# Kernel optimization log

Measured on AMD Instinct MI355X. Metric: run time of the kernel, lower is better.

Reference implementation:

```python
import jax, jax.numpy as jnp
import numpy as np

B, C, H, W = 16, 512, 32, 32
G = 8  # GroupNorm groups
EPS = 1e-5


def setup_inputs() -> dict:
    key = jax.random.key(0)
    ks = jax.random.split(key, 6)
    s = 1.0 / np.sqrt(C)
    return {
        "x": jax.random.normal(ks[0], (B, C, H, W), jnp.float32),
        "gamma": jnp.ones((C,), jnp.float32),
        "beta": jnp.zeros((C,), jnp.float32),
        "wq": jax.random.normal(ks[1], (C, C), jnp.float32) * s,
        "bq": jnp.zeros((C,), jnp.float32),
        "wk": jax.random.normal(ks[2], (C, C), jnp.float32) * s,
        "bk": jnp.zeros((C,), jnp.float32),
        "wv": jax.random.normal(ks[3], (C, C), jnp.float32) * s,
        "bv": jnp.zeros((C,), jnp.float32),
        "wp": jax.random.normal(ks[4], (C, C), jnp.float32) * s,
        "bp": jnp.zeros((C,), jnp.float32),
    }


def reference(x, gamma, beta, wq, bq, wk, bk, wv, bv, wp, bp):
    b, c, h, w = x.shape
    n = h * w
    # GroupNorm(8, C) over (C//G, H, W) per group
    xg = x.reshape(b, G, c // G, n)
    mean = xg.mean(axis=(2, 3), keepdims=True)
    var = xg.var(axis=(2, 3), keepdims=True)
    xn = ((xg - mean) * jax.lax.rsqrt(var + EPS)).reshape(b, c, n)
    xn = xn * gamma[:, None] + beta[:, None]
    # 1x1 conv projections: [C_out, C_in] @ [B, C_in, N]
    q = jnp.einsum('oc,bcn->bon', wq, xn) + bq[:, None]
    k = jnp.einsum('oc,bcn->bon', wk, xn) + bk[:, None]
    v = jnp.einsum('oc,bcn->bon', wv, xn) + bv[:, None]
    scale = 1.0 / (c ** 0.5)
    attn = jax.nn.softmax(jnp.einsum('bci,bcj->bij', q, k) * scale, axis=-1)
    # out[b,c,i] = sum_j v[b,c,j] * attn[b,i,j]
    out = jnp.einsum('bcj,bij->bci', v, attn)
    out = jnp.einsum('oc,bcn->bon', wp, out) + bp[:, None]
    return x + out.reshape(b, c, h, w)
```

## Files before the change

### kernel.cpp

```cpp
#include <hip/hip_runtime.h>

typedef __attribute__((ext_vector_type(8))) short short8;
typedef __attribute__((ext_vector_type(4))) short short4v;
typedef __attribute__((ext_vector_type(4))) float f32x4;
typedef __attribute__((ext_vector_type(4))) int i32x4;

__device__ __forceinline__ short f2bf(float f) {
  unsigned u = __builtin_bit_cast(unsigned, f);
  u = u + 0x7fffu + ((u >> 16) & 1u);
  return (short)(u >> 16);
}
__device__ __forceinline__ int q8(float v) {
  int q = (int)rintf(v * 16.f);
  return q < -127 ? -127 : (q > 127 ? 127 : q);
}
__device__ __forceinline__ int qw8(float v) {
  int q = (int)rintf(v * 512.f);
  return q < -127 ? -127 : (q > 127 ? 127 : q);
}

__device__ __forceinline__ int xcd_swz() {
  const int cpx = gridDim.x >> 3;
  return (blockIdx.x & 7) * cpx + (blockIdx.x >> 3);
}

__global__ __launch_bounds__(256) void pre_kernel(
    const float* __restrict__ x, float2* __restrict__ part,
    const float* __restrict__ wq, const float* __restrict__ wk,
    const float* __restrict__ wp, const float* __restrict__ wv,
    const float* __restrict__ bv, const float* __restrict__ bp,
    short* __restrict__ wp_bf, short* __restrict__ wvT,
    short* __restrict__ wqT, short* __restrict__ wkT,
    float* __restrict__ bias2, float* __restrict__ lsum,
    float* __restrict__ cadd) {
  const int blk = blockIdx.x, t = threadIdx.x;
  if (blk < 32) {
    const int w = t >> 6, lane = t & 63;
    const float4 b0 = *(const float4*)(bv + lane * 8);
    const float4 b1 = *(const float4*)(bv + lane * 8 + 4);
#pragma unroll
    for (int idx = 0; idx < 4; ++idx) {
      const int m = blk * 16 + w * 4 + idx;
      const float4 a0 = *(const float4*)(wp + (long)m * 512 + lane * 8);
      const float4 a1 = *(const float4*)(wp + (long)m * 512 + lane * 8 + 4);
      float s = a0.x * b0.x + a0.y * b0.y + a0.z * b0.z + a0.w * b0.w
              + a1.x * b1.x + a1.y * b1.y + a1.z * b1.z + a1.w * b1.w;
#pragma unroll
      for (int o = 32; o > 0; o >>= 1) s += __shfl_xor(s, o, 64);
      if (lane == 0) bias2[m] = bp[m] + s;
    }
  } else if (blk < 224) {
    const float* src; short* dst; int t2;
    if (blk < 96)       { t2 = blk - 32;  src = wv; dst = wvT; }
    else if (blk < 160) { t2 = blk - 96;  src = wq; dst = wqT; }
    else                { t2 = blk - 160; src = wk; dst = wkT; }
    const int tr = t2 >> 3, tc = t2 & 7;
    __shared__ float tile[64][65];
    const int r = t >> 2, q4 = t & 3;
    const float* s4 = src + (long)(tr * 64 + r) * 512 + tc * 64 + q4 * 16;
#pragma unroll
    for (int k = 0; k < 4; ++k) {
      float4 v = ((const float4*)s4)[k];
      tile[r][q4 * 16 + k * 4 + 0] = v.x;
      tile[r][q4 * 16 + k * 4 + 1] = v.y;
      tile[r][q4 * 16 + k * 4 + 2] = v.z;
      tile[r][q4 * 16 + k * 4 + 3] = v.w;
    }
    __syncthreads();
    const int oc = t >> 2, seg = t & 3;
    short tmp[16];
#pragma unroll
    for (int e = 0; e < 16; ++e) tmp[e] = f2bf(tile[seg * 16 + e][oc]);
    short* dp = dst + (long)(tc * 64 + oc) * 512 + tr * 64 + seg * 16;
    *(short8*)dp = *(short8*)&tmp[0];
    *(short8*)(dp + 8) = *(short8*)&tmp[8];
  } else if (blk < 228) {
    float4* p = (float4*)lsum;
    const int base = (blk - 224) * 1024 + t * 4;
#pragma unroll
    for (int k = 0; k < 4; ++k) p[base + k] = make_float4(0.f, 0.f, 0.f, 0.f);
  } else if (blk < 232) {
    float4* p = (float4*)cadd;
    const int base = (blk - 228) * 1024 + t * 4;
#pragma unroll
    for (int k = 0; k < 4; ++k) p[base + k] = make_float4(0.f, 0.f, 0.f, 0.f);
  } else if (blk < 488) {
    const int i4 = (blk - 232) * 1024 + t * 4;
    float4 v = *(const float4*)(wp + i4);
    short4v o;
    o.x = f2bf(v.x); o.y = f2bf(v.y); o.z = f2bf(v.z); o.w = f2bf(v.w);
    *(short4v*)(wp_bf + i4) = o;
  } else {
    const int blk2 = blk - 488;
    const float* base = x + (long)blk2 * 8192;
    float s = 0.f, ss = 0.f;
#pragma unroll
    for (int j = 0; j < 8; ++j) {
      float4 v = ((const float4*)base)[t + j * 256];
      s  += v.x + v.y + v.z + v.w;
      ss += v.x * v.x + v.y * v.y + v.z * v.z + v.w * v.w;
    }
    for (int o = 32; o > 0; o >>= 1) { s += __shfl_xor(s, o, 64); ss += __shfl_xor(ss, o, 64); }
    __shared__ float rs[4], rss[4];
    if ((t & 63) == 0) { rs[t >> 6] = s; rss[t >> 6] = ss; }
    __syncthreads();
    if (t == 0) {
      part[blk2] = make_float2(rs[0] + rs[1] + rs[2] + rs[3],
                               rss[0] + rss[1] + rss[2] + rss[3]);
    }
  }
}

#define BM 128
#define BK 64

__device__ __forceinline__ int swz_idx(int row, int k) {
  return row * 64 + ((((k >> 3) ^ row) & 7) << 3) + (k & 7);
}

__device__ __forceinline__ void gemm_core(
    const short* __restrict__ Ab, const short* __restrict__ Bb,
    short* lds, f32x4 (&acc)[4][4], int m0, int n0, int K, int tid) {
  const int lane = tid & 63, w = tid >> 6;
  const int wm = (w >> 1) * 64, wn = (w & 1) * 64;
  const int rowst = w * 32 + (lane >> 3);
  for (int k0 = 0; k0 < K; k0 += BK) {
    __syncthreads();
#pragma unroll
    for (int it = 0; it < 4; ++it) {
      int ci = w * 4 + it;
      int row = rowst + it * 8;
      int slot = (lane & 7) ^ (row & 7);
      const short* ga = Ab + (long)(m0 + row) * K + k0 + slot * 8;
      __builtin_amdgcn_global_load_lds(
          (const __attribute__((address_space(1))) void*)ga,
          (__attribute__((address_space(3))) void*)(lds + ci * 512), 16, 0, 0);
      const short* gb = Bb + (long)(n0 + row) * K + k0 + slot * 8;
      __builtin_amdgcn_global_load_lds(
          (const __attribute__((address_space(1))) void*)gb,
          (__attribute__((address_space(3))) void*)(lds + 8192 + ci * 512), 16, 0, 0);
    }
    __syncthreads();
#pragma unroll
    for (int kk = 0; kk < 2; ++kk) {
      short8 af[4], bf[4];
      const int kf = kk * 32 + (lane >> 4) * 8;
#pragma unroll
      for (int i = 0; i < 4; ++i) {
        af[i] = *(const short8*)(lds + swz_idx(wm + i * 16 + (lane & 15), kf));
        bf[i] = *(const short8*)(lds + 8192 + swz_idx(wn + i * 16 + (lane & 15), kf));
      }
#pragma unroll
      for (int i = 0; i < 4; ++i)
#pragma unroll
        for (int j = 0; j < 4; ++j)
          acc[i][j] = __builtin_amdgcn_mfma_f32_16x16x32_bf16(af[i], bf[j], acc[i][j], 0, 0, 0);
    }
  }
}

__device__ __forceinline__ void gemm_core_i8(
    const char* __restrict__ Ab, const char* __restrict__ Bb,
    char* lds, i32x4 (&acc)[4][4], int m0, int n0, int ldaB, int Kbytes, int tid) {
  const int lane = tid & 63, w = tid >> 6;
  const int wm = (w >> 1) * 64, wn = (w & 1) * 64;
  long aoff[4], boff[4];
  int ldst[4];
#pragma unroll
  for (int it = 0; it < 4; ++it) {
    const int ci = w * 4 + it;
    const int row = ci * 8 + (lane >> 3);
    const int lg = (lane & 7) ^ (row & 7);
    aoff[it] = (long)(m0 + row) * ldaB + lg * 16;
    boff[it] = (long)(n0 + row) * ldaB + lg * 16;
    ldst[it] = ci * 1024 + lane * 16;
  }
  const int ar = lane & 15, g4 = lane >> 4;
  for (int k0 = 0; k0 < Kbytes; k0 += 128) {
    __syncthreads();
#pragma unroll
    for (int it = 0; it < 4; ++it) {
      __builtin_amdgcn_global_load_lds(
          (const __attribute__((address_space(1))) void*)(Ab + aoff[it] + k0),
          (__attribute__((address_space(3))) void*)(lds + ldst[it]), 16, 0, 0);
      __builtin_amdgcn_global_load_lds(
          (const __attribute__((address_space(1))) void*)(Bb + boff[it] + k0),
          (__attribute__((address_space(3))) void*)(lds + 16384 + ldst[it]), 16, 0, 0);
    }
    __syncthreads();
#pragma unroll
    for (int kk = 0; kk < 2; ++kk) {
      i32x4 af[4], bf[4];
#pragma unroll
      for (int i = 0; i < 4; ++i) {
        const int rowA = wm + i * 16 + ar;
        af[i] = *(const i32x4*)(lds + rowA * 128 + (((kk * 4 + g4) ^ (rowA & 7)) * 16));
        const int rowB = wn + i * 16 + ar;
        bf[i] = *(const i32x4*)(lds + 16384 + rowB * 128 + (((kk * 4 + g4) ^ (rowB & 7)) * 16));
      }
#pragma unroll
      for (int i = 0; i < 4; ++i)
#pragma unroll
        for (int j = 0; j < 4; ++j)
          acc[i][j] = __builtin_amdgcn_mfma_i32_16x16x64_i8(af[i], bf[j], acc[i][j], 0, 0, 0);
    }
  }
}

__device__ __forceinline__ void gemm_core_fp8(
    const char* __restrict__ Ab, const char* __restrict__ Bb,
    char* lds, f32x4 (&acc)[4][4], int m0, int n0, int ldaB, int Kbytes, int tid) {
  const int lane = tid & 63, w = tid >> 6;
  const int wm = (w >> 1) * 64, wn = (w & 1) * 64;
  long aoff[4], boff[4];
  int ldst[4];
#pragma unroll
  for (int it = 0; it < 4; ++it) {
    const int ci = w * 4 + it;
    const int row = ci * 8 + (lane >> 3);
    const int lg = (lane & 7) ^ (row & 7);
    aoff[it] = (long)(m0 + row) * ldaB + lg * 16;
    boff[it] = (long)(n0 + row) * ldaB + lg * 16;
    ldst[it] = ci * 1024 + lane * 16;
  }
  const int ar = lane & 15, g4 = lane >> 4;
  const int gsel = g4 >> 1, hsel = (g4 & 1) * 8;
  for (int k0 = 0; k0 < Kbytes; k0 += 128) {
    __syncthreads();
#pragma unroll
    for (int it = 0; it < 4; ++it) {
      __builtin_amdgcn_global_load_lds(
          (const __attribute__((address_space(1))) void*)(Ab + aoff[it] + k0),
          (__attribute__((address_space(3))) void*)(lds + ldst[it]), 16, 0, 0);
      __builtin_amdgcn_global_load_lds(
          (const __attribute__((address_space(1))) void*)(Bb + boff[it] + k0),
          (__attribute__((address_space(3))) void*)(lds + 16384 + ldst[it]), 16, 0, 0);
    }
    __syncthreads();
#pragma unroll
    for (int c = 0; c < 4; ++c) {
      long af[4], bf[4];
#pragma unroll
      for (int i = 0; i < 4; ++i) {
        const int rowA = wm + i * 16 + ar;
        af[i] = *(const long*)(lds + rowA * 128 + (((2 * c + gsel) ^ (rowA & 7)) * 16) + hsel);
        const int rowB = wn + i * 16 + ar;
        bf[i] = *(const long*)(lds + 16384 + rowB * 128 + (((2 * c + gsel) ^ (rowB & 7)) * 16) + hsel);
      }
#pragma unroll
      for (int i = 0; i < 4; ++i)
#pragma unroll
        for (int j = 0; j < 4; ++j)
          acc[i][j] = __builtin_amdgcn_mfma_f32_16x16x32_fp8_fp8(af[i], bf[j], acc[i][j], 0, 0, 0);
    }
  }
}

__global__ __launch_bounds__(256, 3) void wgemm_kernel(
    const short* __restrict__ wqT, const short* __restrict__ wkT,
    const short* __restrict__ wp_bf, const short* __restrict__ wvT,
    const float* __restrict__ bq, char* __restrict__ Wst_i8,
    float* __restrict__ v1) {
  __shared__ short lds[2 * BM * BK];
  const int y = blockIdx.y, tid = threadIdx.x;
  if (y < 8) {
    const int which = y >> 2;
    const short* A  = which ? wp_bf : wqT;
    const short* Bt = which ? wvT   : wkT;
    const int m0 = (y & 3) * 128, n0 = blockIdx.x * 128;
    f32x4 acc[4][4] = {};
    gemm_core(A, Bt, lds, acc, m0, n0, 512, tid);
    const int lane = tid & 63, w = tid >> 6;
    const int wm = (w >> 1) * 64, wn = (w & 1) * 64;
    const int mb = m0 + wm + (lane >> 4) * 4;
    const int nb = n0 + wn + (lane & 15);
    char* C = Wst_i8 + which * 262144;
#pragma unroll
    for (int i = 0; i < 4; ++i)
#pragma unroll
      for (int r = 0; r < 4; ++r) {
        int m = mb + i * 16 + r;
#pragma unroll
        for (int j = 0; j < 4; ++j)
          C[(long)m * 512 + nb + j * 16] = (char)qw8(acc[i][j][r]);
      }
  } else {
    const int w = tid >> 6, lane = tid & 63;
    const int base_r = ((y - 8) * 4 + blockIdx.x) * 64;
    const float4 b0 = *(const float4*)(bq + lane * 8);
    const float4 b1 = *(const float4*)(bq + lane * 8 + 4);
#pragma unroll
    for (int idx = 0; idx < 16; ++idx) {
      const int c = base_r + w * 16 + idx;
      const short8 a = *(const short8*)(wkT + (long)c * 512 + lane * 8);
      float av[8];
#pragma unroll
      for (int e = 0; e < 8; ++e)
        av[e] = __builtin_bit_cast(float, ((unsigned)(unsigned short)a[e]) << 16);
      float s = av[0] * b0.x + av[1] * b0.y + av[2] * b0.z + av[3] * b0.w
              + av[4] * b1.x + av[5] * b1.y + av[6] * b1.z + av[7] * b1.w;
#pragma unroll
      for (int o = 32; o > 0; o >>= 1) s += __shfl_xor(s, o, 64);
      if (lane == 0) v1[c] = s;
    }
  }
}

#define TP 133
__global__ __launch_bounds__(256) void gn_norm_t(
    const float* __restrict__ x, const float2* __restrict__ part,
    const float* __restrict__ gamma, const float* __restrict__ beta,
    const float* __restrict__ v1, char* __restrict__ xi8,
    float* __restrict__ cadd) {
  const int blk = blockIdx.x;
  const int nc = blk & 7, g = (blk >> 3) & 7, b = blk >> 6;
  const int t = threadIdx.x;
  float s = 0.f, ss = 0.f;
#pragma unroll
  for (int j = 0; j < 8; ++j) {
    float2 p = part[(b * 8 + g) * 8 + j];
    s += p.x; ss += p.y;
  }
  const float mean = s * (1.f / 65536.f);
  const float var  = ss * (1.f / 65536.f) - mean * mean;
  const float rstd = rsqrtf(var + 1e-5f);

  const float* base = x + (long)(b * 512 + g * 64) * 1024 + nc * 128;
  __shared__ float tile[64][TP];
  const int row = t >> 2, c4 = t & 3;
#pragma unroll
  for (int j = 0; j < 8; ++j) {
    float4 v = *(const float4*)(base + (long)row * 1024 + (c4 + j * 4) * 4);
    *(float4*)&tile[row][(c4 + j * 4) * 4] = v;
  }
  const int cl4 = (t & 15) * 4;
  float ga[4], be[4];
#pragma unroll
  for (int j = 0; j < 4; ++j) {
    float gm = gamma[g * 64 + cl4 + j];
    ga[j] = gm * rstd;
    be[j] = beta[g * 64 + cl4 + j] - mean * ga[j];
  }
  const float4 v1c = *(const float4*)(v1 + g * 64 + cl4);
  __syncthreads();
  char* qb = xi8 + (long)b * 524288 + (long)(nc * 128) * 512 + g * 64 + cl4;
  float* cb = cadd + b * 1024 + nc * 128;
#pragma unroll
  for (int it = 0; it < 8; ++it) {
    const int tok = (t >> 4) + it * 16;
    float x0 = tile[cl4 + 0][tok] * ga[0] + be[0];
    float x1 = tile[cl4 + 1][tok] * ga[1] + be[1];
    float x2 = tile[cl4 + 2][tok] * ga[2] + be[2];
    float x3 = tile[cl4 + 3][tok] * ga[3] + be[3];
    unsigned pk = (q8(x0) & 255) | ((q8(x1) & 255) << 8)
                | ((q8(x2) & 255) << 16) | ((q8(x3) & 255) << 24);
    *(unsigned*)(qb + (long)tok * 512) = pk;
    float p = v1c.x * x0 + v1c.y * x1 + v1c.z * x2 + v1c.w * x3;
    p += __shfl_xor(p, 1, 64); p += __shfl_xor(p, 2, 64);
    p += __shfl_xor(p, 4, 64); p += __shfl_xor(p, 8, 64);
    if ((t & 15) == 0) atomicAdd(&cb[tok], p);
  }
}

__global__ __launch_bounds__(256, 3) void zu_gemm(
    const char* __restrict__ Wst_i8, const char* __restrict__ xi,
    char* __restrict__ zi, char* __restrict__ u8) {
  __shared__ char lds[32768];
  const int lw = xcd_swz();
  const int b = lw >> 6, rem = lw & 63, y = rem >> 3, xg = rem & 7;
  const int which = y >> 2;
  const int m0 = y * 128;
  const int mloc0 = m0 - which * 512;
  const int n0 = xg * 128;
  const char* Bb = xi + (long)b * 524288;
  const int tid = threadIdx.x, lane = tid & 63;
  i32x4 acc[4][4] = {};
  gemm_core_i8(Wst_i8, Bb, lds, acc, m0, n0, 512, 512, tid);

  const int w = tid >> 6;
  const int wm = (w >> 1) * 64, wn = (w & 1) * 64;
  const int mb = mloc0 + wm + (lane >> 4) * 4;
  const int nb = n0 + wn + (lane & 15);
  const float dq = 1.f / 8192.f;
  if (which == 0) {
    char* C = zi + (long)b * 524288;
#pragma unroll
    for (int i = 0; i < 4; ++i) {
      int m = mb + i * 16;
#pragma unroll
      for (int j = 0; j < 4; ++j) {
        int n = nb + j * 16;
        unsigned pk = (q8((float)acc[i][j][0] * dq) & 255)
                    | ((q8((float)acc[i][j][1] * dq) & 255) << 8)
                    | ((q8((float)acc[i][j][2] * dq) & 255) << 16)
                    | ((q8((float)acc[i][j][3] * dq) & 255) << 24);
        *(unsigned*)(C + (long)n * 512 + m) = pk;
      }
    }
  } else {
    char* C = u8 + (long)b * 524288;
#pragma unroll
    for (int i = 0; i < 4; ++i) {
#pragma unroll
      for (int r = 0; r < 4; ++r) {
        int m = mb + i * 16 + r;
#pragma unroll
        for (int j = 0; j < 4; ++j) {
          int n = nb + j * 16;
          float v = (float)acc[i][j][r] * dq;
          int pk = __builtin_amdgcn_cvt_pk_fp8_f32(v, v, 0, false);
          C[(long)m * 1024 + n] = (char)(pk & 255);
        }
      }
    }
  }
}

__global__ __launch_bounds__(256, 3) void sexp_i8(
    const char* __restrict__ zi, const char* __restrict__ xi,
    char* __restrict__ P8, float* __restrict__ lsum,
    const float* __restrict__ cadd, float scale) {
  __shared__ char lds[32768];
  const int lw = xcd_swz();
  const int b = lw >> 6, rem = lw & 63;
  const int m0 = (rem >> 3) * 128, n0 = (rem & 7) * 128;
  const char* Ab = zi + (long)b * 524288;
  const char* Bb = xi + (long)b * 524288;
  const int tid = threadIdx.x, lane = tid & 63, w = tid >> 6;
  const int wm = (w >> 1) * 64, wn = (w & 1) * 64;
  i32x4 acc[4][4] = {};
  gemm_core_i8(Ab, Bb, lds, acc, m0, n0, 512, 512, tid);

  const int ar = lane & 15, g4 = lane >> 4;
  const int mb = m0 + wm + g4 * 4;
  const int nb = n0 + wn + ar;
  char* C = P8 + (long)b * 1048576;
  float4 ca[4];
#pragma unroll
  for (int i = 0; i < 4; ++i)
    ca[i] = *(const float4*)(cadd + b * 1024 + mb + i * 16);
  float rowsum[4] = {0.f, 0.f, 0.f, 0.f};
  const float qs = 1.f / 256.f;
#pragma unroll
  for (int j = 0; j < 4; ++j) {
    int n = nb + j * 16;
#pragma unroll
    for (int i = 0; i < 4; ++i) {
      int m = mb + i * 16;
      float e0 = __expf(((float)acc[i][j][0] * qs + ca[i].x) * scale);
      float e1 = __expf(((float)acc[i][j][1] * qs + ca[i].y) * scale);
      float e2 = __expf(((float)acc[i][j][2] * qs + ca[i].z) * scale);
      float e3 = __expf(((float)acc[i][j][3] * qs + ca[i].w) * scale);
      rowsum[j] += (e0 + e1) + (e2 + e3);
      int pk = __builtin_amdgcn_cvt_pk_fp8_f32(e0, e1, 0, false);
      pk = __builtin_amdgcn_cvt_pk_fp8_f32(e2, e3, pk, true);
      *(unsigned*)(C + (long)n * 1024 + m) = (unsigned)pk;
    }
  }
#pragma unroll
  for (int j = 0; j < 4; ++j) {
    rowsum[j] += __shfl_xor(rowsum[j], 16, 64);
    rowsum[j] += __shfl_xor(rowsum[j], 32, 64);
  }
  if (lane < 16) {
#pragma unroll
    for (int j = 0; j < 4; ++j)
      atomicAdd(&lsum[b * 1024 + nb + j * 16], rowsum[j]);
  }
}

__global__ __launch_bounds__(256, 3) void out_fp8(
    const char* __restrict__ u8, const char* __restrict__ P8,
    float* __restrict__ out, const float* __restrict__ bias2,
    const float* __restrict__ x, const float* __restrict__ lsum) {
  __shared__ char lds[32768];
  const int lw = xcd_swz();
  const int b = lw >> 5, rem = lw & 31;
  const int m0 = (rem >> 3) * 128, n0 = (rem & 7) * 128;
  const char* Ab = u8 + (long)b * 524288;
  const char* Bb = P8 + (long)b * 1048576;
  const int tid = threadIdx.x, lane = tid & 63, w = tid >> 6;
  const int wm = (w >> 1) * 64, wn = (w & 1) * 64;
  f32x4 acc[4][4] = {};
  gemm_core_fp8(Ab, Bb, lds, acc, m0, n0, 1024, 1024, tid);

  const int ar = lane & 15, g4 = lane >> 4;
  const int mb = m0 + wm + g4 * 4;
  const int nb = n0 + wn + ar;
  float* C = out + (long)b * 524288;
  const float* R = x + (long)b * 524288;
#pragma unroll
  for (int j = 0; j < 4; ++j) {
    int n = nb + j * 16;
    float rl = 1.0f / lsum[b * 1024 + n];
#pragma unroll
    for (int i = 0; i < 4; ++i) {
#pragma unroll
      for (int r = 0; r < 4; ++r) {
        int m = mb + i * 16 + r;
        C[(long)m * 1024 + n] = acc[i][j][r] * rl + bias2[m] + R[(long)m * 1024 + n];
      }
    }
  }
}

extern "C" void kernel_launch(void* const* d_in, const int* in_sizes, int n_in,
                              void* d_out, int out_size, void* d_ws, size_t ws_size,
                              hipStream_t stream) {
  const float* x     = (const float*)d_in[0];
  const float* gamma = (const float*)d_in[1];
  const float* beta  = (const float*)d_in[2];
  const float* wq    = (const float*)d_in[3];
  const float* bq    = (const float*)d_in[4];
  const float* wk    = (const float*)d_in[5];
  const float* bk    = (const float*)d_in[6];
  const float* wv    = (const float*)d_in[7];
  const float* bv    = (const float*)d_in[8];
  const float* wp    = (const float*)d_in[9];
  const float* bp    = (const float*)d_in[10];
  (void)bk;

  char* ws = (char*)d_ws;
  char*  Wst_i8 = (char*)ws;
  float* bias2 = (float*)(ws + 1572864l);
  float* lsum  = (float*)(ws + 1638400l);
  float* v1    = (float*)(ws + 1703936l);
  float* cadd  = (float*)(ws + 1708032l);
  char*  z_i8  = (char*)(ws + 18874368l);
  char*  x_i8  = (char*)(ws + 35651584l);
  char*  u_f8  = (char*)(ws + 52428800l);
  char*  P8    = (char*)(ws + 69206016l);
  float2* gnpart = (float2*)P8;
  short* wp_bf = (short*)(P8 + 131072);
  short* wvT   = (short*)(P8 + 655360);
  short* wqT   = (short*)(P8 + 1179648);
  short* wkT   = (short*)(P8 + 1703936);

  pre_kernel<<<1512, 256, 0, stream>>>(
      x, gnpart, wq, wk, wp, wv, bv, bp, wp_bf, wvT, wqT, wkT,
      bias2, lsum, cadd);

  wgemm_kernel<<<dim3(4, 10), 256, 0, stream>>>(
      wqT, wkT, wp_bf, wvT, bq, Wst_i8, v1);

  gn_norm_t<<<1024, 256, 0, stream>>>(
      x, gnpart, gamma, beta, v1, x_i8, cadd);

  zu_gemm<<<1024, 256, 0, stream>>>(Wst_i8, x_i8, z_i8, u_f8);

  const float iscale = 0.044194173824159216f;
  sexp_i8<<<1024, 256, 0, stream>>>(z_i8, x_i8, P8, lsum, cadd, iscale);

  out_fp8<<<512, 256, 0, stream>>>(u_f8, P8, (float*)d_out, bias2, x, lsum);
}
```

Before: 100.2 us.

## Load int8 GEMM operands directly from global into registers, bypassing LDS

Replaces the LDS-staged int8 GEMM core (global_load_lds plus two barriers per K step) with a version where each wave loads its MFMA fragments straight from global memory into registers, fully unrolled over K. Both zu_gemm and sexp_i8 drop their shared memory buffers and the occupancy hint in launch_bounds. This removes barrier and LDS round-trip overhead, but gives up cross-wave reuse of tiles, so each operand row is fetched by two waves and relies on L2/L1 caching. The full unroll also raises register pressure.

```diff
diff --git a/kernel.cpp b/kernel.cpp
--- a/kernel.cpp
+++ b/kernel.cpp
@@ -159,51 +159,32 @@
   }
 }
 
-__device__ __forceinline__ void gemm_core_i8(
+__device__ __forceinline__ void gemm_core_i8_reg(
     const char* __restrict__ Ab, const char* __restrict__ Bb,
-    char* lds, i32x4 (&acc)[4][4], int m0, int n0, int ldaB, int Kbytes, int tid) {
+    i32x4 (&acc)[4][4], int m0, int n0, int ldaB, int Kbytes, int tid) {
   const int lane = tid & 63, w = tid >> 6;
   const int wm = (w >> 1) * 64, wn = (w & 1) * 64;
-  long aoff[4], boff[4];
-  int ldst[4];
-#pragma unroll
-  for (int it = 0; it < 4; ++it) {
-    const int ci = w * 4 + it;
-    const int row = ci * 8 + (lane >> 3);
-    const int lg = (lane & 7) ^ (row & 7);
-    aoff[it] = (long)(m0 + row) * ldaB + lg * 16;
-    boff[it] = (long)(n0 + row) * ldaB + lg * 16;
-    ldst[it] = ci * 1024 + lane * 16;
-  }
   const int ar = lane & 15, g4 = lane >> 4;
-  for (int k0 = 0; k0 < Kbytes; k0 += 128) {
-    __syncthreads();
-#pragma unroll
-    for (int it = 0; it < 4; ++it) {
-      __builtin_amdgcn_global_load_lds(
-          (const __attribute__((address_space(1))) void*)(Ab + aoff[it] + k0),
-          (__attribute__((address_space(3))) void*)(lds + ldst[it]), 16, 0, 0);
-      __builtin_amdgcn_global_load_lds(
-          (const __attribute__((address_space(1))) void*)(Bb + boff[it] + k0),
-          (__attribute__((address_space(3))) void*)(lds + 16384 + ldst[it]), 16, 0, 0);
-    }
-    __syncthreads();
-#pragma unroll
-    for (int kk = 0; kk < 2; ++kk) {
-      i32x4 af[4], bf[4];
-#pragma unroll
-      for (int i = 0; i < 4; ++i) {
-        const int rowA = wm + i * 16 + ar;
-        af[i] = *(const i32x4*)(lds + rowA * 128 + (((kk * 4 + g4) ^ (rowA & 7)) * 16));
-        const int rowB = wn + i * 16 + ar;
-        bf[i] = *(const i32x4*)(lds + 16384 + rowB * 128 + (((kk * 4 + g4) ^ (rowB & 7)) * 16));
-      }
-#pragma unroll
-      for (int i = 0; i < 4; ++i)
-#pragma unroll
-        for (int j = 0; j < 4; ++j)
-          acc[i][j] = __builtin_amdgcn_mfma_i32_16x16x64_i8(af[i], bf[j], acc[i][j], 0, 0, 0);
-    }
+  const char* arow[4];
+  const char* brow[4];
+#pragma unroll
+  for (int i = 0; i < 4; ++i) {
+    arow[i] = Ab + (long)(m0 + wm + i * 16 + ar) * ldaB + g4 * 16;
+    brow[i] = Bb + (long)(n0 + wn + i * 16 + ar) * ldaB + g4 * 16;
+  }
+#pragma unroll
+  for (int ks = 0; ks < Kbytes; ks += 64) {
+    i32x4 af[4], bf[4];
+#pragma unroll
+    for (int i = 0; i < 4; ++i) {
+      af[i] = *(const i32x4*)(arow[i] + ks);
+      bf[i] = *(const i32x4*)(brow[i] + ks);
+    }
+#pragma unroll
+    for (int i = 0; i < 4; ++i)
+#pragma unroll
+      for (int j = 0; j < 4; ++j)
+        acc[i][j] = __builtin_amdgcn_mfma_i32_16x16x64_i8(af[i], bf[j], acc[i][j], 0, 0, 0);
   }
 }
 
@@ -362,10 +343,9 @@
   }
 }
 
-__global__ __launch_bounds__(256, 3) void zu_gemm(
+__global__ __launch_bounds__(256) void zu_gemm(
     const char* __restrict__ Wst_i8, const char* __restrict__ xi,
     char* __restrict__ zi, char* __restrict__ u8) {
-  __shared__ char lds[32768];
   const int lw = xcd_swz();
   const int b = lw >> 6, rem = lw & 63, y = rem >> 3, xg = rem & 7;
   const int which = y >> 2;
@@ -375,7 +355,7 @@
   const char* Bb = xi + (long)b * 524288;
   const int tid = threadIdx.x, lane = tid & 63;
   i32x4 acc[4][4] = {};
-  gemm_core_i8(Wst_i8, Bb, lds, acc, m0, n0, 512, 512, tid);
+  gemm_core_i8_reg(Wst_i8, Bb, acc, m0, n0, 512, 512, tid);
 
   const int w = tid >> 6;
   const int wm = (w >> 1) * 64, wn = (w & 1) * 64;
@@ -416,11 +396,10 @@
   }
 }
 
-__global__ __launch_bounds__(256, 3) void sexp_i8(
+__global__ __launch_bounds__(256) void sexp_i8(
     const char* __restrict__ zi, const char* __restrict__ xi,
     char* __restrict__ P8, float* __restrict__ lsum,
     const float* __restrict__ cadd, float scale) {
-  __shared__ char lds[32768];
   const int lw = xcd_swz();
   const int b = lw >> 6, rem = lw & 63;
   const int m0 = (rem >> 3) * 128, n0 = (rem & 7) * 128;
@@ -429,7 +408,7 @@
   const int tid = threadIdx.x, lane = tid & 63, w = tid >> 6;
   const int wm = (w >> 1) * 64, wn = (w & 1) * 64;
   i32x4 acc[4][4] = {};
-  gemm_core_i8(Ab, Bb, lds, acc, m0, n0, 512, 512, tid);
+  gemm_core_i8_reg(Ab, Bb, acc, m0, n0, 512, 512, tid);
 
   const int ar = lane & 15, g4 = lane >> 4;
   const int mb = m0 + wm + g4 * 4;
```

New measurement: 135.8 us. 1.36x slower.
